# Performance work log

Hardware: AMD Instinct MI355X
Metric: run time of the kernel (lower is better)

Reference implementation:

```python
import jax, jax.numpy as jnp
import numpy as np

N_NODES = 50000
N_REL = 4
N_EDGES = 400000
IN_F, HID_F, OUT_F = 128, 128, 64


def _graphconv(h, s, d, W, b, n_nodes):
    """DGL GraphConv, norm='both': D_dst^{-1/2} A D_src^{-1/2} h W + b.
    Degrees clamped to min 1 (DGL behavior for isolated nodes)."""
    ones = jnp.ones(s.shape[0], h.dtype)
    deg_out = jnp.clip(jax.ops.segment_sum(ones, s, num_segments=n_nodes), 1.0)
    deg_in = jnp.clip(jax.ops.segment_sum(ones, d, num_segments=n_nodes), 1.0)
    # scale src features, transform first (weight applied pre-aggregation)
    hw = (h * jax.lax.rsqrt(deg_out)[:, None]) @ W          # [N, out]
    msg = hw[s]                                              # gather  [E, out]
    agg = jax.ops.segment_sum(msg, d, num_segments=n_nodes)  # scatter [N, out]
    return agg * jax.lax.rsqrt(deg_in)[:, None] + b


def _hetero_layer(h, src, dst, W, b):
    # HeteroGraphConv with aggregate='sum': sum per-relation GraphConv outputs
    n_nodes = h.shape[0]
    out = _graphconv(h, src[0], dst[0], W[0], b[0], n_nodes)
    for r in range(1, W.shape[0]):
        out = out + _graphconv(h, src[r], dst[r], W[r], b[r], n_nodes)
    return out


def setup_inputs() -> dict:
    key = jax.random.key(0)
    k = jax.random.split(key, 6)
    x = jax.random.normal(k[0], (N_NODES, IN_F), dtype=jnp.float32)
    src = jax.random.randint(k[1], (N_REL, N_EDGES), 0, N_NODES, dtype=jnp.int32)
    dst = jax.random.randint(k[2], (N_REL, N_EDGES), 0, N_NODES, dtype=jnp.int32)
    W1 = jax.random.normal(k[3], (N_REL, IN_F, HID_F), dtype=jnp.float32) / np.sqrt(IN_F)
    b1 = jnp.zeros((N_REL, HID_F), dtype=jnp.float32)
    W2 = jax.random.normal(k[4], (N_REL, HID_F, OUT_F), dtype=jnp.float32) / np.sqrt(HID_F)
    b2 = jnp.zeros((N_REL, OUT_F), dtype=jnp.float32)
    return {"x": x, "src": src, "dst": dst, "W1": W1, "b1": b1, "W2": W2, "b2": b2}


def reference(x, src, dst, W1, b1, W2, b2):
    h = _hetero_layer(x, src, dst, W1, b1)
    h = jax.nn.relu(h)
    return _hetero_layer(h, src, dst, W2, b2)
```

## Files before the change

### kernel.cpp

```cpp
#include <hip/hip_runtime.h>
#include <hip/hip_bf16.h>

#define N_NODES 50000
#define N_REL 4
#define N_EDGES 400000
#define CHUNK 1024
#define NCHUNK ((N_NODES + CHUNK - 1) / CHUNK)

#define EB 32
#define ECH (N_EDGES / EB)
#define NR 8
#define RNG (N_NODES / NR)

#define PX_BLOCKS 3125
#define PW_BLOCKS 192
#define HIST_BLOCKS (N_REL * EB * NR)

#define G1_BLOCKS 1563

using short8 = __attribute__((ext_vector_type(8))) short;
using f32x4 = __attribute__((ext_vector_type(4))) float;

static __device__ inline unsigned short f2bf(float f) {
  unsigned u = __float_as_uint(f);
  unsigned r = (u + 0x7FFFu + ((u >> 16) & 1u)) >> 16;
  return (unsigned short)r;
}
static __device__ inline float bf2f(unsigned short b) {
  return __uint_as_float(((unsigned)b) << 16);
}
static __device__ inline void fma_bf2(unsigned w, float ds, float& a0,
                                      float& a1) {
  float lo = __uint_as_float(w << 16);
  float hi = __uint_as_float(w & 0xffff0000u);
  a0 = fmaf(lo, ds, a0);
  a1 = fmaf(hi, ds, a1);
}

__global__ __launch_bounds__(256) void k_prep_fused(
    const float* __restrict__ x, const float* __restrict__ W1,
    const float* __restrict__ W2, const int* __restrict__ src,
    const int* __restrict__ dst, unsigned short* __restrict__ xb,
    unsigned short* __restrict__ Wt1, unsigned short* __restrict__ Wt2,
    unsigned short* __restrict__ Hs, unsigned short* __restrict__ Hd,
    int* __restrict__ chunkSums) {
  __shared__ unsigned int ldsS[RNG / 2], ldsD[RNG / 2];
  const int b = blockIdx.x;
  const int tid = threadIdx.x;
  if (b < PX_BLOCKS) {
    if (b == 0 && tid < 64) chunkSums[tid] = 0;
    int i = b * 256 + tid;
    const float4* p = (const float4*)x + (size_t)i * 2;
    float4 v0 = p[0], v1 = p[1];
    unsigned short pk[8] = {f2bf(v0.x), f2bf(v0.y), f2bf(v0.z), f2bf(v0.w),
                            f2bf(v1.x), f2bf(v1.y), f2bf(v1.z), f2bf(v1.w)};
    *(uint4*)(xb + (size_t)i * 8) = *(uint4*)pk;
    return;
  }
  if (b < PX_BLOCKS + PW_BLOCKS) {
    int ob = (b - PX_BLOCKS) * 2 + (tid >> 7);
    int kk = tid & 127;
    if (ob < 128) {
      int c = ob;
#pragma unroll
      for (int r = 0; r < 4; ++r)
        Wt1[(size_t)c * 512 + r * 128 + kk] =
            f2bf(W1[(size_t)r * 16384 + kk * 128 + c]);
    } else {
      int c = ob - 128;
      int r = c >> 6, cc = c & 63;
      Wt2[(size_t)c * 128 + kk] = f2bf(W2[(size_t)r * 8192 + kk * 64 + cc]);
    }
    return;
  }
  const int hb = b - PX_BLOCKS - PW_BLOCKS;
  const int range = hb % NR;
  const int chunk = (hb / NR) % EB;
  const int rel = hb / (NR * EB);
  for (int i = tid; i < RNG / 2; i += 256) {
    ldsS[i] = 0u;
    ldsD[i] = 0u;
  }
  __syncthreads();
  const int n0 = range * RNG;
  const int* sp = src + (size_t)rel * N_EDGES + chunk * ECH;
  const int* dp = dst + (size_t)rel * N_EDGES + chunk * ECH;
  for (int e = tid; e < ECH; e += 256) {
    int s = sp[e] - n0;
    if ((unsigned)s < RNG) atomicAdd(&ldsS[s >> 1], 1u << ((s & 1) * 16));
    int d = dp[e] - n0;
    if ((unsigned)d < RNG) atomicAdd(&ldsD[d >> 1], 1u << ((d & 1) * 16));
  }
  __syncthreads();
  unsigned int* HsO =
      (unsigned int*)(Hs + ((size_t)rel * EB + chunk) * N_NODES + n0);
  unsigned int* HdO =
      (unsigned int*)(Hd + ((size_t)rel * EB + chunk) * N_NODES + n0);
  for (int i = tid; i < RNG / 2; i += 256) {
    HsO[i] = ldsS[i];
    HdO[i] = ldsD[i];
  }
}

__global__ __launch_bounds__(256) void k_reduce_m(
    const unsigned short* __restrict__ Hs, unsigned short* __restrict__ Hd,
    int* __restrict__ cnt_m, float* __restrict__ dso, float* __restrict__ dsi,
    ushort4* __restrict__ relOff, int* __restrict__ chunkSums) {
  int n = blockIdx.x * 256 + threadIdx.x;
  int run = 0;
  if (n < N_NODES) {
#pragma unroll
    for (int r = 0; r < N_REL; ++r) {
      int so = 0;
#pragma unroll
      for (int b = 0; b < EB; ++b)
        so += Hs[((size_t)r * EB + b) * N_NODES + n];
      dso[r * N_NODES + n] = rsqrtf((float)(so < 1 ? 1 : so));
    }
    unsigned short rs[4];
#pragma unroll
    for (int r = 0; r < N_REL; ++r) {
      rs[r] = (unsigned short)run;
#pragma unroll
      for (int b = 0; b < EB; ++b) {
        size_t off = ((size_t)r * EB + b) * N_NODES + n;
        int v = Hd[off];
        Hd[off] = (unsigned short)run;
        run += v;
      }
      int di = run - rs[r];
      dsi[r * N_NODES + n] = rsqrtf((float)(di < 1 ? 1 : di));
    }
    cnt_m[n] = run;
    relOff[n] = make_ushort4(rs[0], rs[1], rs[2], rs[3]);
  }
  __shared__ int red[256];
  red[threadIdx.x] = run;
  __syncthreads();
  for (int off = 128; off > 0; off >>= 1) {
    if (threadIdx.x < off) red[threadIdx.x] += red[threadIdx.x + off];
    __syncthreads();
  }
  if (threadIdx.x == 0) atomicAdd(&chunkSums[blockIdx.x >> 2], red[0]);
}

__global__ __launch_bounds__(64) void k_scan_chunks(int* __restrict__ chunkSums,
                                                    int* __restrict__ row_ptr) {
  if (threadIdx.x == 0) {
    int running = 0;
    for (int c = 0; c < NCHUNK; ++c) {
      int v = chunkSums[c];
      chunkSums[c] = running;
      running += v;
    }
    row_ptr[N_NODES] = N_REL * N_EDGES;
  }
}

__global__ __launch_bounds__(256) void k_scan_within(
    const int* __restrict__ cnt_m, const int* __restrict__ chunkOff,
    int* __restrict__ row_ptr) {
  int c = blockIdx.x;
  int t = threadIdx.x;
  int base = c * CHUNK + t * 4;
  int v[4];
#pragma unroll
  for (int j = 0; j < 4; ++j) {
    int n = base + j;
    v[j] = (n < N_NODES) ? cnt_m[n] : 0;
  }
  int total = v[0] + v[1] + v[2] + v[3];
  __shared__ int lds[256];
  lds[t] = total;
  __syncthreads();
  for (int off = 1; off < 256; off <<= 1) {
    int add = (t >= off) ? lds[t - off] : 0;
    __syncthreads();
    lds[t] += add;
    __syncthreads();
  }
  int thrExcl = lds[t] - total + chunkOff[c];
  int pre = 0;
#pragma unroll
  for (int j = 0; j < 4; ++j) {
    int n = base + j;
    if (n < N_NODES) row_ptr[n] = thrExcl + pre;
    pre += v[j];
  }
}

__global__ __launch_bounds__(256) void k_fill2m(
    const int* __restrict__ src, const int* __restrict__ dst,
    const unsigned short* __restrict__ Hd, const int* __restrict__ row_ptr,
    int* __restrict__ sorted) {
  const int range = blockIdx.x % NR;
  const int chunk = (blockIdx.x / NR) % EB;
  const int rel = blockIdx.x / (NR * EB);
  __shared__ unsigned int cur[RNG];
  const int n0 = range * RNG;
  const int* rp = row_ptr + n0;
  const unsigned short* pref = Hd + ((size_t)rel * EB + chunk) * N_NODES + n0;
  for (int i = threadIdx.x; i < RNG; i += 256)
    cur[i] = (unsigned)(rp[i] + pref[i]);
  __syncthreads();
  const int* sp = src + (size_t)rel * N_EDGES + chunk * ECH;
  const int* dp = dst + (size_t)rel * N_EDGES + chunk * ECH;
  for (int e = threadIdx.x; e < ECH; e += 256) {
    int d = dp[e] - n0;
    if ((unsigned)d < RNG) {
      unsigned pos = atomicAdd(&cur[d], 1u);
      sorted[pos] = sp[e];
    }
  }
}

__global__ __launch_bounds__(256) void k_gather1a(
    const unsigned short* __restrict__ xb, const int* __restrict__ row_ptr,
    const ushort4* __restrict__ relOff, const int* __restrict__ sortedm,
    const float* __restrict__ dso, const float* __restrict__ dsi,
    unsigned int* __restrict__ agg) {
  const int fq = blockIdx.x / G1_BLOCKS;
  const int nb = blockIdx.x % G1_BLOCKS;
  const int wave = threadIdx.x >> 6, lane = threadIdx.x & 63;
  const int g = lane & 7;
  const int node = nb * 32 + wave * 8 + (lane >> 3);
  if (node >= N_NODES) return;
  const int rp = row_ptr[node], rp1 = row_ptr[node + 1];
  const ushort4 ro = relOff[node];
  const int beg[4] = {rp + ro.x, rp + ro.y, rp + ro.z, rp + ro.w};
  const int end4[4] = {rp + ro.y, rp + ro.z, rp + ro.w, rp1};
  const unsigned short* xq = xb + fq * 32 + g * 4;
#pragma unroll
  for (int r = 0; r < 4; ++r) {
    const float* dsoR = dso + (size_t)r * N_NODES;
    float a0[4] = {0, 0, 0, 0}, a1[4] = {0, 0, 0, 0};
    float a2[4] = {0, 0, 0, 0}, a3[4] = {0, 0, 0, 0};
    for (int base = beg[r]; base < end4[r]; base += 8) {
      int n = end4[r] - base;
      if (n > 8) n = 8;
      int my = (g < n) ? sortedm[base + g] : 0;
      int j = 0;
      for (; j + 3 < n; j += 4) {
#pragma unroll
        for (int k = 0; k < 4; ++k) {
          int s = __shfl(my, j + k, 8);
          float ds = dsoR[s];
          uint2 w = *(const uint2*)(xq + (size_t)s * 128);
          fma_bf2(w.x, ds, a0[k], a1[k]);
          fma_bf2(w.y, ds, a2[k], a3[k]);
        }
      }
      for (; j < n; ++j) {
        int s = __shfl(my, j, 8);
        float ds = dsoR[s];
        uint2 w = *(const uint2*)(xq + (size_t)s * 128);
        fma_bf2(w.x, ds, a0[0], a1[0]);
        fma_bf2(w.y, ds, a2[0], a3[0]);
      }
    }
    float di = dsi[(size_t)r * N_NODES + node];
    float t0 = ((a0[0] + a0[1]) + (a0[2] + a0[3])) * di;
    float t1 = ((a1[0] + a1[1]) + (a1[2] + a1[3])) * di;
    float t2 = ((a2[0] + a2[1]) + (a2[2] + a2[3])) * di;
    float t3 = ((a3[0] + a3[1]) + (a3[2] + a3[3])) * di;
    uint2 pk;
    pk.x = (unsigned)f2bf(t0) | ((unsigned)f2bf(t1) << 16);
    pk.y = (unsigned)f2bf(t2) | ((unsigned)f2bf(t3) << 16);
    *((uint2*)agg + ((size_t)node * 4 + r) * 32 + fq * 8 + g) = pk;
  }
}

__global__ __launch_bounds__(256, 2) void k_gemm_h1(
    const unsigned short* __restrict__ agg, const unsigned short* __restrict__ Wt,
    const float* __restrict__ b1, unsigned short* __restrict__ h1, int M) {
  __shared__ unsigned short Alds[64 * 128];
  __shared__ unsigned short Wlds[128 * 128];
  const int tid = threadIdx.x;
  const int wid = tid >> 6, lane = tid & 63;
  const int rowBase = blockIdx.x * 64;
  const int lrow = lane & 15;
  const int quarter = lane >> 4;

  f32x4 acc[4][2];
#pragma unroll
  for (int i = 0; i < 4; ++i)
#pragma unroll
    for (int j = 0; j < 2; ++j) acc[i][j] = (f32x4){0.f, 0.f, 0.f, 0.f};

  for (int k0 = 0; k0 < 4; ++k0) {
    __syncthreads();
#pragma unroll
    for (int it = 0; it < 4; ++it) {
      int cid = tid + it * 256;
      int row = cid >> 4, kg = cid & 15;
      int grow = rowBase + row;
      uint4 v = make_uint4(0, 0, 0, 0);
      if (grow < M)
        v = *(const uint4*)(agg + (size_t)grow * 512 + k0 * 128 + kg * 8);
      *(uint4*)(Alds + row * 128 + ((kg ^ (row & 7)) * 8)) = v;
    }
#pragma unroll
    for (int it = 0; it < 8; ++it) {
      int cid = tid + it * 256;
      int c = cid >> 4, kg = cid & 15;
      uint4 v = *(const uint4*)(Wt + (size_t)c * 512 + k0 * 128 + kg * 8);
      *(uint4*)(Wlds + c * 128 + ((kg ^ (c & 7)) * 8)) = v;
    }
    __syncthreads();
#pragma unroll
    for (int kk = 0; kk < 4; ++kk) {
      int kg = kk * 4 + quarter;
      short8 a[4], b[2];
#pragma unroll
      for (int i = 0; i < 4; ++i) {
        int row = i * 16 + lrow;
        a[i] = *(const short8*)(Alds + row * 128 + ((kg ^ (row & 7)) * 8));
      }
#pragma unroll
      for (int j = 0; j < 2; ++j) {
        int c = wid * 32 + j * 16 + lrow;
        b[j] = *(const short8*)(Wlds + c * 128 + ((kg ^ (c & 7)) * 8));
      }
#pragma unroll
      for (int i = 0; i < 4; ++i)
#pragma unroll
        for (int j = 0; j < 2; ++j)
          acc[i][j] = __builtin_amdgcn_mfma_f32_16x16x32_bf16(a[i], b[j],
                                                              acc[i][j], 0, 0, 0);
    }
  }

#pragma unroll
  for (int j = 0; j < 2; ++j) {
    int c = wid * 32 + j * 16 + lrow;
    float bs = b1[c] + b1[128 + c] + b1[256 + c] + b1[384 + c];
#pragma unroll
    for (int i = 0; i < 4; ++i) {
#pragma unroll
      for (int r = 0; r < 4; ++r) {
        int grow = rowBase + i * 16 + quarter * 4 + r;
        if (grow < M)
          h1[(size_t)grow * 128 + c] = f2bf(fmaxf(acc[i][j][r] + bs, 0.f));
      }
    }
  }
}

template <int REL_COLS>
__global__ __launch_bounds__(256, 2) void k_gemm_mfma(
    const unsigned short* __restrict__ A, const unsigned short* __restrict__ Wt,
    const float* __restrict__ dsoBase, unsigned short* __restrict__ C,
    int cstride, int M) {
  __shared__ unsigned short Alds[64 * 128];
  __shared__ unsigned short Wlds[256 * 128];
  const int tid = threadIdx.x;
  const int wid = tid >> 6, lane = tid & 63;
  const int rowBase = blockIdx.x * 64;

#pragma unroll
  for (int i = 0; i < 4; ++i) {
    int cid = tid + i * 256;
    int row = cid >> 4, kg = cid & 15;
    int grow = rowBase + row;
    uint4 v = make_uint4(0, 0, 0, 0);
    if (grow < M) v = *(const uint4*)(A + (size_t)grow * 128 + kg * 8);
    *(uint4*)(Alds + row * 128 + ((kg ^ (row & 7)) * 8)) = v;
  }
#pragma unroll
  for (int i = 0; i < 16; ++i) {
    int cid = tid + i * 256;
    int row = cid >> 4, kg = cid & 15;
    uint4 v = *(const uint4*)(Wt + (size_t)row * 128 + kg * 8);
    *(uint4*)(Wlds + row * 128 + ((kg ^ (row & 7)) * 8)) = v;
  }
  __syncthreads();

  f32x4 acc[4][4];
#pragma unroll
  for (int i = 0; i < 4; ++i)
#pragma unroll
    for (int j = 0; j < 4; ++j) acc[i][j] = (f32x4){0.f, 0.f, 0.f, 0.f};

  const int lrow = lane & 15;
  const int khalf = lane >> 4;
#pragma unroll
  for (int k0 = 0; k0 < 4; ++k0) {
    int kg = k0 * 4 + khalf;
    short8 a[4], b[4];
#pragma unroll
    for (int i = 0; i < 4; ++i) {
      int row = i * 16 + lrow;
      a[i] = *(const short8*)(Alds + row * 128 + ((kg ^ (row & 7)) * 8));
    }
#pragma unroll
    for (int j = 0; j < 4; ++j) {
      int wrow = wid * 64 + j * 16 + lrow;
      b[j] = *(const short8*)(Wlds + wrow * 128 + ((kg ^ (wrow & 7)) * 8));
    }
#pragma unroll
    for (int i = 0; i < 4; ++i)
#pragma unroll
      for (int j = 0; j < 4; ++j)
        acc[i][j] = __builtin_amdgcn_mfma_f32_16x16x32_bf16(a[i], b[j],
                                                            acc[i][j], 0, 0, 0);
  }

#pragma unroll
  for (int i = 0; i < 4; ++i) {
#pragma unroll
    for (int j = 0; j < 4; ++j) {
      int col = wid * 64 + j * 16 + (lane & 15);
      const float* dsoCol = dsoBase + (size_t)(col / REL_COLS) * N_NODES;
#pragma unroll
      for (int r = 0; r < 4; ++r) {
        int grow = rowBase + i * 16 + (lane >> 4) * 4 + r;
        if (grow < M)
          C[(size_t)grow * cstride + col] = f2bf(acc[i][j][r] * dsoCol[grow]);
      }
    }
  }
}

__global__ __launch_bounds__(256) void k_gather2m(
    const unsigned short* __restrict__ Y, const int* __restrict__ row_ptr,
    const ushort4* __restrict__ relOff, const int* __restrict__ sortedm,
    const float* __restrict__ dsi, const float* __restrict__ b2,
    float* __restrict__ out) {
  const int wave = threadIdx.x >> 6, lane = threadIdx.x & 63;
  const int g = lane & 15;
  const int node = blockIdx.x * 16 + wave * 4 + (lane >> 4);
  const int rp = row_ptr[node], rp1 = row_ptr[node + 1];
  const ushort4 ro = relOff[node];
  const int beg[4] = {rp + ro.x, rp + ro.y, rp + ro.z, rp + ro.w};
  const int end4[4] = {rp + ro.y, rp + ro.z, rp + ro.w, rp1};
  float t0 = 0.f, t1 = 0.f, t2 = 0.f, t3 = 0.f;
#pragma unroll
  for (int r = 0; r < 4; ++r) {
    float a0[4] = {0, 0, 0, 0}, a1[4] = {0, 0, 0, 0};
    float a2[4] = {0, 0, 0, 0}, a3[4] = {0, 0, 0, 0};
    for (int base = beg[r]; base < end4[r]; base += 16) {
      int n = end4[r] - base;
      if (n > 16) n = 16;
      int my = (g < n) ? sortedm[base + g] : 0;
      int j = 0;
      for (; j + 3 < n; j += 4) {
#pragma unroll
        for (int k = 0; k < 4; ++k) {
          int s = __shfl(my, j + k, 16);
          uint2 w = *(const uint2*)(Y + ((size_t)s * 4 + r) * 64 + g * 4);
          fma_bf2(w.x, 1.f, a0[k], a1[k]);
          fma_bf2(w.y, 1.f, a2[k], a3[k]);
        }
      }
      for (; j < n; ++j) {
        int s = __shfl(my, j, 16);
        uint2 w = *(const uint2*)(Y + ((size_t)s * 4 + r) * 64 + g * 4);
        fma_bf2(w.x, 1.f, a0[0], a1[0]);
        fma_bf2(w.y, 1.f, a2[0], a3[0]);
      }
    }
    float di = dsi[(size_t)r * N_NODES + node];
    t0 = fmaf((a0[0] + a0[1]) + (a0[2] + a0[3]), di, t0);
    t1 = fmaf((a1[0] + a1[1]) + (a1[2] + a1[3]), di, t1);
    t2 = fmaf((a2[0] + a2[1]) + (a2[2] + a2[3]), di, t2);
    t3 = fmaf((a3[0] + a3[1]) + (a3[2] + a3[3]), di, t3);
  }
#pragma unroll
  for (int r = 0; r < 4; ++r) {
    float4 bb = *(const float4*)(b2 + r * 64 + g * 4);
    t0 += bb.x;
    t1 += bb.y;
    t2 += bb.z;
    t3 += bb.w;
  }
  *(float4*)(out + (size_t)node * 64 + g * 4) = make_float4(t0, t1, t2, t3);
}

extern "C" void kernel_launch(void* const* d_in, const int* in_sizes, int n_in,
                              void* d_out, int out_size, void* d_ws,
                              size_t ws_size, hipStream_t stream) {
  const float* x  = (const float*)d_in[0];
  const int* src  = (const int*)d_in[1];
  const int* dst  = (const int*)d_in[2];
  const float* W1 = (const float*)d_in[3];
  const float* b1 = (const float*)d_in[4];
  const float* W2 = (const float*)d_in[5];
  const float* b2 = (const float*)d_in[6];
  float* out = (float*)d_out;

  char* wsb = (char*)d_ws;
  unsigned short* Hs = (unsigned short*)wsb;
  unsigned short* h1 = (unsigned short*)wsb;
  unsigned short* Hd = Hs + (size_t)N_REL * EB * N_NODES;
  unsigned short* xb = Hd + (size_t)N_REL * EB * N_NODES;
  unsigned short* agg = xb + (size_t)N_NODES * 128;
  unsigned short* Y2 = agg;
  char* tail = (char*)(agg + (size_t)N_NODES * 512);
  unsigned short* Wt1 = (unsigned short*)tail;
  unsigned short* Wt2 = Wt1 + 128 * 512;
  float* dso = (float*)(Wt2 + 256 * 128);
  float* dsi = dso + N_REL * N_NODES;
  ushort4* relOff = (ushort4*)(dsi + N_REL * N_NODES);
  int* cnt_m = (int*)(relOff + N_NODES);
  int* row_ptr = cnt_m + N_NODES;
  int* chunkSums = row_ptr + (N_NODES + 1);
  int* sorted = chunkSums + 64;

  k_prep_fused<<<PX_BLOCKS + PW_BLOCKS + HIST_BLOCKS, 256, 0, stream>>>(
      x, W1, W2, src, dst, xb, Wt1, Wt2, Hs, Hd, chunkSums);
  k_reduce_m<<<(N_NODES + 255) / 256, 256, 0, stream>>>(Hs, Hd, cnt_m, dso,
                                                        dsi, relOff, chunkSums);
  k_scan_chunks<<<1, 64, 0, stream>>>(chunkSums, row_ptr);
  k_scan_within<<<NCHUNK, 256, 0, stream>>>(cnt_m, chunkSums, row_ptr);
  k_fill2m<<<N_REL * EB * NR, 256, 0, stream>>>(src, dst, Hd, row_ptr, sorted);

  k_gather1a<<<4 * G1_BLOCKS, 256, 0, stream>>>(xb, row_ptr, relOff, sorted,
                                                dso, dsi, (unsigned int*)agg);
  k_gemm_h1<<<(N_NODES + 63) / 64, 256, 0, stream>>>(agg, Wt1, b1, h1,
                                                     N_NODES);
  k_gemm_mfma<64><<<(N_NODES + 63) / 64, 256, 0, stream>>>(h1, Wt2, dso, Y2,
                                                           256, N_NODES);
  k_gather2m<<<N_NODES / 16, 256, 0, stream>>>(Y2, row_ptr, relOff, sorted,
                                               dsi, b2, out);
}
```

Before: 320.7 us.

## Store sorted edge sources as uint16 and gather full rows per node

```diff
diff --git a/kernel.cpp b/kernel.cpp
--- a/kernel.cpp
+++ b/kernel.cpp
@@ -15,8 +15,6 @@
 #define PX_BLOCKS 3125
 #define PW_BLOCKS 192
 #define HIST_BLOCKS (N_REL * EB * NR)
-
-#define G1_BLOCKS 1563
 
 using short8 = __attribute__((ext_vector_type(8))) short;
 using f32x4 = __attribute__((ext_vector_type(4))) float;
@@ -192,7 +190,7 @@
 __global__ __launch_bounds__(256) void k_fill2m(
     const int* __restrict__ src, const int* __restrict__ dst,
     const unsigned short* __restrict__ Hd, const int* __restrict__ row_ptr,
-    int* __restrict__ sorted) {
+    unsigned short* __restrict__ sorted) {
   const int range = blockIdx.x % NR;
   const int chunk = (blockIdx.x / NR) % EB;
   const int rel = blockIdx.x / (NR * EB);
@@ -209,51 +207,47 @@
     int d = dp[e] - n0;
     if ((unsigned)d < RNG) {
       unsigned pos = atomicAdd(&cur[d], 1u);
-      sorted[pos] = sp[e];
+      sorted[pos] = (unsigned short)sp[e];
     }
   }
 }
 
 __global__ __launch_bounds__(256) void k_gather1a(
     const unsigned short* __restrict__ xb, const int* __restrict__ row_ptr,
-    const ushort4* __restrict__ relOff, const int* __restrict__ sortedm,
+    const ushort4* __restrict__ relOff, const unsigned short* __restrict__ sortedm,
     const float* __restrict__ dso, const float* __restrict__ dsi,
     unsigned int* __restrict__ agg) {
-  const int fq = blockIdx.x / G1_BLOCKS;
-  const int nb = blockIdx.x % G1_BLOCKS;
   const int wave = threadIdx.x >> 6, lane = threadIdx.x & 63;
-  const int g = lane & 7;
-  const int node = nb * 32 + wave * 8 + (lane >> 3);
-  if (node >= N_NODES) return;
+  const int g = lane & 31;
+  const int node = blockIdx.x * 8 + wave * 2 + (lane >> 5);
   const int rp = row_ptr[node], rp1 = row_ptr[node + 1];
   const ushort4 ro = relOff[node];
   const int beg[4] = {rp + ro.x, rp + ro.y, rp + ro.z, rp + ro.w};
   const int end4[4] = {rp + ro.y, rp + ro.z, rp + ro.w, rp1};
-  const unsigned short* xq = xb + fq * 32 + g * 4;
 #pragma unroll
   for (int r = 0; r < 4; ++r) {
     const float* dsoR = dso + (size_t)r * N_NODES;
     float a0[4] = {0, 0, 0, 0}, a1[4] = {0, 0, 0, 0};
     float a2[4] = {0, 0, 0, 0}, a3[4] = {0, 0, 0, 0};
-    for (int base = beg[r]; base < end4[r]; base += 8) {
+    for (int base = beg[r]; base < end4[r]; base += 32) {
       int n = end4[r] - base;
-      if (n > 8) n = 8;
-      int my = (g < n) ? sortedm[base + g] : 0;
+      if (n > 32) n = 32;
+      int my = (g < n) ? (int)sortedm[base + g] : 0;
       int j = 0;
       for (; j + 3 < n; j += 4) {
 #pragma unroll
         for (int k = 0; k < 4; ++k) {
-          int s = __shfl(my, j + k, 8);
+          int s = __shfl(my, j + k, 32);
           float ds = dsoR[s];
-          uint2 w = *(const uint2*)(xq + (size_t)s * 128);
+          uint2 w = *(const uint2*)(xb + (size_t)s * 128 + g * 4);
           fma_bf2(w.x, ds, a0[k], a1[k]);
           fma_bf2(w.y, ds, a2[k], a3[k]);
         }
       }
       for (; j < n; ++j) {
-        int s = __shfl(my, j, 8);
+        int s = __shfl(my, j, 32);
         float ds = dsoR[s];
-        uint2 w = *(const uint2*)(xq + (size_t)s * 128);
+        uint2 w = *(const uint2*)(xb + (size_t)s * 128 + g * 4);
         fma_bf2(w.x, ds, a0[0], a1[0]);
         fma_bf2(w.y, ds, a2[0], a3[0]);
       }
@@ -266,7 +260,7 @@
     uint2 pk;
     pk.x = (unsigned)f2bf(t0) | ((unsigned)f2bf(t1) << 16);
     pk.y = (unsigned)f2bf(t2) | ((unsigned)f2bf(t3) << 16);
-    *((uint2*)agg + ((size_t)node * 4 + r) * 32 + fq * 8 + g) = pk;
+    *((uint2*)agg + ((size_t)node * 4 + r) * 32 + g) = pk;
   }
 }
 
@@ -423,7 +417,7 @@
 
 __global__ __launch_bounds__(256) void k_gather2m(
     const unsigned short* __restrict__ Y, const int* __restrict__ row_ptr,
-    const ushort4* __restrict__ relOff, const int* __restrict__ sortedm,
+    const ushort4* __restrict__ relOff, const unsigned short* __restrict__ sortedm,
     const float* __restrict__ dsi, const float* __restrict__ b2,
     float* __restrict__ out) {
   const int wave = threadIdx.x >> 6, lane = threadIdx.x & 63;
@@ -441,7 +435,7 @@
     for (int base = beg[r]; base < end4[r]; base += 16) {
       int n = end4[r] - base;
       if (n > 16) n = 16;
-      int my = (g < n) ? sortedm[base + g] : 0;
+      int my = (g < n) ? (int)sortedm[base + g] : 0;
       int j = 0;
       for (; j + 3 < n; j += 4) {
 #pragma unroll
@@ -504,7 +498,7 @@
   int* cnt_m = (int*)(relOff + N_NODES);
   int* row_ptr = cnt_m + N_NODES;
   int* chunkSums = row_ptr + (N_NODES + 1);
-  int* sorted = chunkSums + 64;
+  unsigned short* sorted = (unsigned short*)(chunkSums + 64);
 
   k_prep_fused<<<PX_BLOCKS + PW_BLOCKS + HIST_BLOCKS, 256, 0, stream>>>(
       x, W1, W2, src, dst, xb, Wt1, Wt2, Hs, Hd, chunkSums);
@@ -514,8 +508,8 @@
   k_scan_within<<<NCHUNK, 256, 0, stream>>>(cnt_m, chunkSums, row_ptr);
   k_fill2m<<<N_REL * EB * NR, 256, 0, stream>>>(src, dst, Hd, row_ptr, sorted);
 
-  k_gather1a<<<4 * G1_BLOCKS, 256, 0, stream>>>(xb, row_ptr, relOff, sorted,
-                                                dso, dsi, (unsigned int*)agg);
+  k_gather1a<<<N_NODES / 8, 256, 0, stream>>>(xb, row_ptr, relOff, sorted, dso,
+                                              dsi, (unsigned int*)agg);
   k_gemm_h1<<<(N_NODES + 63) / 64, 256, 0, stream>>>(agg, Wt1, b1, h1,
                                                      N_NODES);
   k_gemm_mfma<64><<<(N_NODES + 63) / 64, 256, 0, stream>>>(h1, Wt2, dso, Y2,
```

New measurement: 267.1 us. -16.7%, faster.
